# Kernel tuning notes

Measured on AMD Instinct MI355X. Metric: run time of the kernel, lower is better.

The kernel has to match this reference:

```python
import jax, jax.numpy as jnp
import numpy as np

# Junction-tree config: chain of NC cliques, each owning K new variables,
# parent separator = previous clique's K vars; S states per var; MLP hidden H.
B, NC, K, S, H = 512, 512, 4, 8, 128
D = 2 * K * S


def setup_inputs() -> dict:
    key = jax.random.key(0)
    ks = jax.random.split(key, 4)
    x = jax.random.randint(ks[0], (B, NC * K), 0, S, dtype=jnp.int32)
    sc = 0.05
    W1 = jax.random.normal(ks[1], (NC, D, H), jnp.float32) * sc
    b1 = jnp.zeros((NC, H), jnp.float32)
    W2 = jax.random.normal(ks[2], (NC, H, H), jnp.float32) * sc
    b2 = jnp.zeros((NC, H), jnp.float32)
    W3 = jax.random.normal(ks[3], (NC, H, S), jnp.float32) * sc
    b3 = jnp.zeros((NC, S), jnp.float32)
    return dict(x=x, W1=W1, b1=b1, W2=W2, b2=b2, W3=W3, b3=b3)


def reference(x, W1, b1, W2, b2, W3, b3):
    """fast_likelihood: per-clique log-prob [B, NC].

    Clique i owns vars [i*K,(i+1)*K); parent of clique i is clique i-1 (root=0
    conditions on a zero parent vector). Each clique runs a conditional
    autoregressive MLP over its K variables.
    """
    dtype = W1.dtype
    Bx = x.shape[0]
    xc = x.reshape(Bx, NC, K)                         # [B,NC,K] clique states
    oh = jax.nn.one_hot(xc, S, dtype=dtype)           # [B,NC,K,S]
    # Parent separator one-hot (root clique gets zeros) -> gather along tree.
    parent = jnp.concatenate([jnp.zeros_like(oh[:, :1]), oh[:, :-1]], axis=1)
    parent_flat = parent.reshape(Bx, NC, K * S)       # [B,NC,K*S]
    prefix_mask = (jnp.arange(K)[:, None] > jnp.arange(K)[None, :]).astype(dtype)  # [Kpos,Kvar]
    prefix = jnp.einsum('jk,bnks->bnjks', prefix_mask, oh).reshape(Bx, NC, K, K * S)
    inp = jnp.concatenate(
        [jnp.broadcast_to(parent_flat[:, :, None], prefix.shape), prefix], axis=-1
    )                                                 # [B,NC,K,D]
    h = jax.nn.relu(jnp.einsum('bnkd,ndh->bnkh', inp, W1) + b1[None, :, None])
    h = jax.nn.relu(jnp.einsum('bnkh,nhg->bnkg', h, W2) + b2[None, :, None])
    logits = jnp.einsum('bnkh,nhs->bnks', h, W3) + b3[None, :, None]
    logp = jax.nn.log_softmax(logits, axis=-1)        # [B,NC,K,S]
    logp_obs = jnp.take_along_axis(logp, xc[..., None], axis=-1)[..., 0]  # [B,NC,K]
    return logp_obs.sum(axis=-1)                      # [B,NC] per-clique logps
```

## Files before the change

kernel.cpp:

```cpp
#include <hip/hip_runtime.h>
#include <hip/hip_bf16.h>

typedef __bf16 bf16;
typedef __attribute__((ext_vector_type(4)))  __bf16 bf16x4;
typedef __attribute__((ext_vector_type(8)))  __bf16 bf16x8;
typedef __attribute__((ext_vector_type(16))) float  f32x16;

#define B_   512
#define NC_  512
#define K_   4
#define S_   8
#define H_   128
#define D_   64
#define XROW (NC_ * K_)
#define NITER 32

static __device__ __forceinline__ int swap23(int v) {
    return (v & ~12) | ((v & 4) << 1) | ((v & 8) >> 1);
}

__global__ __launch_bounds__(256, 2)
void jt_mlp_kernel(const int*   __restrict__ x,
                   const float* __restrict__ W1g, const float* __restrict__ b1g,
                   const float* __restrict__ W2g, const float* __restrict__ b2g,
                   const float* __restrict__ W3g, const float* __restrict__ b3g,
                   float* __restrict__ out)
{
    __shared__ __align__(16) bf16 SW2[128 * 128];
    __shared__ __align__(16) bf16 SWX[128 * 64];
    __shared__ __align__(16) bf16 SW3[8 * 128];
    __shared__ __align__(16) float LX[2][64][4];

    const int tid  = threadIdx.x;
    const int lane = tid & 63;
    const int w    = tid >> 6;
    const int pair = w >> 1;
    const int h    = w & 1;
    const int l31  = lane & 31;
    const int lhi  = lane >> 5;
    const int kk   = l31 & 3;
    const int n    = blockIdx.x;

    const float* W1p = W1g + (size_t)n * (D_ * H_);
    const float* W2p = W2g + (size_t)n * (H_ * H_);
    const float* W3p = W3g + (size_t)n * (H_ * S_);
    const float* b1p = b1g + n * H_;
    const float* b2p = b2g + n * H_;
    const float* b3p = b3g + n * S_;

    const int p31 = swap23(l31);
    const bf16 one = (bf16)1.0f, zero = (bf16)0.0f;

    {
        const int c0 = (tid & 31) * 4;
        const int k0 = (tid >> 5) * 8;
        float rows[8][4];
#pragma unroll
        for (int i = 0; i < 8; ++i) {
            float4 t4 = *(const float4*)(W1p + (k0 + i) * H_ + c0);
            if (n == 0 && k0 < 32) t4 = make_float4(0.f, 0.f, 0.f, 0.f);
            rows[i][0] = t4.x; rows[i][1] = t4.y; rows[i][2] = t4.z; rows[i][3] = t4.w;
        }
        if (k0 == 0) {
            const float4 bb = *(const float4*)(b1p + c0);
#pragma unroll
            for (int i = 0; i < 8; ++i) {
                rows[i][0] += bb.x; rows[i][1] += bb.y;
                rows[i][2] += bb.z; rows[i][3] += bb.w;
            }
        }
#pragma unroll
        for (int j2 = 0; j2 < 4; ++j2) {
            const int c = c0 + j2;
            const int p = (c & ~31) | swap23(c & 31);
            const int ch = (k0 >> 3) ^ (p & 7);
            bf16x4 lo, hi;
#pragma unroll
            for (int i = 0; i < 4; ++i) {
                lo[i] = (bf16)rows[i][j2];
                hi[i] = (bf16)rows[4 + i][j2];
            }
            *(bf16x4*)&SWX[p * 64 + ch * 8 + 0] = lo;
            *(bf16x4*)&SWX[p * 64 + ch * 8 + 4] = hi;
        }
    }
    {
        const int c0 = (tid & 31) * 4;
        const int kbase = (tid >> 5) * 16;
#pragma unroll
        for (int hh = 0; hh < 2; ++hh) {
            const int k0 = kbase + hh * 8;
            float rows[8][4];
#pragma unroll
            for (int i = 0; i < 8; ++i) {
                const float4 t4 = *(const float4*)(W2p + (k0 + i) * H_ + c0);
                rows[i][0] = t4.x; rows[i][1] = t4.y; rows[i][2] = t4.z; rows[i][3] = t4.w;
            }
#pragma unroll
            for (int j2 = 0; j2 < 4; ++j2) {
                const int c = c0 + j2;
                const int p = (c & ~31) | swap23(c & 31);
                const int ch = (k0 >> 3) ^ (p & 15) ^ ((p & 16) >> 2);
                bf16x4 lo, hi;
#pragma unroll
                for (int i = 0; i < 4; ++i) {
                    lo[i] = (bf16)rows[i][j2];
                    hi[i] = (bf16)rows[4 + i][j2];
                }
                *(bf16x4*)&SW2[p * 128 + ch * 8 + 0] = lo;
                *(bf16x4*)&SW2[p * 128 + ch * 8 + 4] = hi;
            }
        }
    }
    if (tid < 128) {
        const int s = tid >> 4, kc = tid & 15, k0 = kc * 8;
        float vv[8];
#pragma unroll
        for (int i = 0; i < 8; ++i) vv[i] = W3p[(k0 + i) * S_ + s];
        const int ch = kc ^ s;
        bf16x4 lo, hi;
#pragma unroll
        for (int i = 0; i < 4; ++i) { lo[i] = (bf16)vv[i]; hi[i] = (bf16)vv[4 + i]; }
        *(bf16x4*)&SW3[s * 128 + ch * 8 + 0] = lo;
        *(bf16x4*)&SW3[s * 128 + ch * 8 + 4] = hi;
    }
    __syncthreads();

    bf16x8 w1f[2][4];
#pragma unroll
    for (int aa = 0; aa < 2; ++aa)
#pragma unroll
        for (int kt = 0; kt < 4; ++kt)
            w1f[aa][kt] = *(const bf16x8*)
                &SWX[(32 * (2 * h + aa) + l31) * 64 + (((kt << 1) + lhi) ^ (l31 & 7)) * 8];
    const int s2 = l31 & 7;
    bf16x8 w3f[4];
#pragma unroll
    for (int tt = 0; tt < 4; ++tt)
        w3f[tt] = *(const bf16x8*)
            &SW3[s2 * 128 + ((((4 * h + tt) << 1) + lhi) ^ s2) * 8];
    bf16x8 w2b0, w2b1, onef;
#pragma unroll
    for (int j = 0; j < 8; ++j) { w2b0[j] = zero; w2b1[j] = zero; onef[j] = zero; }
    w2b0[0] = lhi ? zero : (bf16)b2p[32 * (2 * h + 0) + p31];
    w2b1[0] = lhi ? zero : (bf16)b2p[32 * (2 * h + 1) + p31];
    onef[0] = lhi ? zero : one;
    const float4 b3q = *(const float4*)(b3p + 4 * lhi);

    f32x16 zf;
#pragma unroll
    for (int i = 0; i < 16; ++i) zf[i] = 0.f;

    __syncthreads();
    bf16* HX = SWX;

    const int itbase = pair * 256 + (l31 >> 2);
    int4 xo_c, xp_c;
    {
        const int* xb = x + (size_t)itbase * XROW + n * K_;
        xo_c = *(const int4*)xb;
        xp_c = (n > 0) ? *(const int4*)(xb - K_) : make_int4(0, 0, 0, 0);
    }

#pragma unroll 1
    for (int c = 0; c < NITER; ++c) {
        const int item = itbase + c * 8;
        const int4 xo = xo_c, xp = xp_c;
        if (c < NITER - 1) {
            const int* xb = x + (size_t)(item + 8) * XROW + n * K_;
            xo_c = *(const int4*)xb;
            xp_c = (n > 0) ? *(const int4*)(xb - K_) : make_int4(0, 0, 0, 0);
        }

        int sel[4];
        sel[0] = (n > 0) ? (lhi ? xp.y : xp.x) : (lhi ? -1 : 0);
        sel[1] = (n > 0) ? (lhi ? xp.w : xp.z) : -1;
        sel[2] = (kk > (lhi ? 1 : 0)) ? (lhi ? xo.y : xo.x) : -1;
        sel[3] = (kk > (lhi ? 3 : 2)) ? (lhi ? xo.w : xo.z) : -1;

        f32x16 A0 = zf, A1 = zf;
#pragma unroll
        for (int kt = 0; kt < 4; ++kt) {
            bf16x8 bf1;
#pragma unroll
            for (int j = 0; j < 8; ++j) bf1[j] = (sel[kt] == j) ? one : zero;
            A0 = __builtin_amdgcn_mfma_f32_32x32x16_bf16(w1f[0][kt], bf1, A0, 0, 0, 0);
            A1 = __builtin_amdgcn_mfma_f32_32x32x16_bf16(w1f[1][kt], bf1, A1, 0, 0, 0);
        }

        bf16x8 hfo[4];
#pragma unroll
        for (int t = 0; t < 4; ++t) {
            const f32x16& S = (t < 2) ? A0 : A1;
#pragma unroll
            for (int j = 0; j < 8; ++j)
                hfo[t][j] = (bf16)fmaxf(S[8 * (t & 1) + j], 0.f);
            *(bf16x8*)&HX[(((pair << 1) + h) * 4 + t) * 512 + lane * 8] = hfo[t];
        }
        __syncthreads();

        f32x16 C0 = zf, C1 = zf;
        const int swz = (l31 & 15) ^ ((l31 & 16) >> 2);
        const int p0 = (64 * h + l31) * 128;
        const int p1 = (64 * h + 32 + l31) * 128;
#pragma unroll
        for (int tt = 0; tt < 4; ++tt) {
            const int chunk = (((4 * h + tt) << 1) + lhi) ^ swz;
            const bf16x8 f0 = *(const bf16x8*)&SW2[p0 + chunk * 8];
            const bf16x8 f1 = *(const bf16x8*)&SW2[p1 + chunk * 8];
            C0 = __builtin_amdgcn_mfma_f32_32x32x16_bf16(f0, hfo[tt], C0, 0, 0, 0);
            C1 = __builtin_amdgcn_mfma_f32_32x32x16_bf16(f1, hfo[tt], C1, 0, 0, 0);
        }
#pragma unroll
        for (int tt = 0; tt < 4; ++tt) {
            const bf16x8 hp = *(const bf16x8*)
                &HX[(((pair << 1) + (1 - h)) * 4 + tt) * 512 + lane * 8];
            const int chunk = (((4 * (1 - h) + tt) << 1) + lhi) ^ swz;
            const bf16x8 f0 = *(const bf16x8*)&SW2[p0 + chunk * 8];
            const bf16x8 f1 = *(const bf16x8*)&SW2[p1 + chunk * 8];
            C0 = __builtin_amdgcn_mfma_f32_32x32x16_bf16(f0, hp, C0, 0, 0, 0);
            C1 = __builtin_amdgcn_mfma_f32_32x32x16_bf16(f1, hp, C1, 0, 0, 0);
        }
        C0 = __builtin_amdgcn_mfma_f32_32x32x16_bf16(w2b0, onef, C0, 0, 0, 0);
        C1 = __builtin_amdgcn_mfma_f32_32x32x16_bf16(w2b1, onef, C1, 0, 0, 0);

        f32x16 L = zf;
#pragma unroll
        for (int tt = 0; tt < 4; ++tt) {
            bf16x8 hg;
            const f32x16& S = (tt < 2) ? C0 : C1;
#pragma unroll
            for (int j = 0; j < 8; ++j)
                hg[j] = (bf16)fmaxf(S[8 * (tt & 1) + j], 0.f);
            L = __builtin_amdgcn_mfma_f32_32x32x16_bf16(w3f[tt], hg, L, 0, 0, 0);
        }

        if (h == 1)
            *(float4*)&LX[pair][lane][0] = make_float4(L[0], L[1], L[2], L[3]);
        __syncthreads();
        if (h == 0) {
            const float4 Lp = *(const float4*)&LX[pair][lane][0];
            float Ls0 = L[0] + Lp.x + b3q.x;
            float Ls1 = L[1] + Lp.y + b3q.y;
            float Ls2 = L[2] + Lp.z + b3q.z;
            float Ls3 = L[3] + Lp.w + b3q.w;

            float m4 = fmaxf(fmaxf(Ls0, Ls1), fmaxf(Ls2, Ls3));
            const float mm = fmaxf(m4, __shfl_xor(m4, 32));
            float e = __expf(Ls0 - mm) + __expf(Ls1 - mm) +
                      __expf(Ls2 - mm) + __expf(Ls3 - mm);
            const float ssum = e + __shfl_xor(e, 32);

            const int xs = (kk & 2) ? ((kk & 1) ? xo.w : xo.z)
                                    : ((kk & 1) ? xo.y : xo.x);
            const float own = (xs & 2) ? ((xs & 1) ? Ls3 : Ls2)
                                       : ((xs & 1) ? Ls1 : Ls0);
            const float oth = __shfl_xor(own, 32);
            const float obs = ((xs >> 2) == lhi) ? own : oth;
            float lp = obs - mm - __logf(ssum);
            lp += __shfl_xor(lp, 1);
            lp += __shfl_xor(lp, 2);
            if (lhi == 0 && kk == 0)
                out[(size_t)item * NC_ + n] = lp;
        }
    }
}

extern "C" void kernel_launch(void* const* d_in, const int* in_sizes, int n_in,
                              void* d_out, int out_size, void* d_ws, size_t ws_size,
                              hipStream_t stream) {
    const int*   x  = (const int*)d_in[0];
    const float* W1 = (const float*)d_in[1];
    const float* b1 = (const float*)d_in[2];
    const float* W2 = (const float*)d_in[3];
    const float* b2 = (const float*)d_in[4];
    const float* W3 = (const float*)d_in[5];
    const float* b3 = (const float*)d_in[6];
    float* out = (float*)d_out;
    jt_mlp_kernel<<<dim3(NC_), 256, 0, stream>>>(x, W1, b1, W2, b2, W3, b3, out);
}
```

Before: 169.7 us.

## Give each wave a full 32-token slice instead of splitting hidden across wave pairs

```diff
diff --git a/kernel.cpp b/kernel.cpp
--- a/kernel.cpp
+++ b/kernel.cpp
@@ -13,7 +13,7 @@
 #define H_   128
 #define D_   64
 #define XROW (NC_ * K_)
-#define NITER 32
+#define NITER 16
 
 static __device__ __forceinline__ int swap23(int v) {
     return (v & ~12) | ((v & 4) << 1) | ((v & 8) >> 1);
@@ -29,13 +29,10 @@
     __shared__ __align__(16) bf16 SW2[128 * 128];
     __shared__ __align__(16) bf16 SWX[128 * 64];
     __shared__ __align__(16) bf16 SW3[8 * 128];
-    __shared__ __align__(16) float LX[2][64][4];
 
     const int tid  = threadIdx.x;
     const int lane = tid & 63;
     const int w    = tid >> 6;
-    const int pair = w >> 1;
-    const int h    = w & 1;
     const int l31  = lane & 31;
     const int lhi  = lane >> 5;
     const int kk   = l31 & 3;
@@ -126,35 +123,33 @@
     }
     __syncthreads();
 
-    bf16x8 w1f[2][4];
-#pragma unroll
-    for (int aa = 0; aa < 2; ++aa)
+    bf16x8 w1f[4][4];
+#pragma unroll
+    for (int aa = 0; aa < 4; ++aa)
 #pragma unroll
         for (int kt = 0; kt < 4; ++kt)
             w1f[aa][kt] = *(const bf16x8*)
-                &SWX[(32 * (2 * h + aa) + l31) * 64 + (((kt << 1) + lhi) ^ (l31 & 7)) * 8];
+                &SWX[(32 * aa + l31) * 64 + (((kt << 1) + lhi) ^ (l31 & 7)) * 8];
+
     const int s2 = l31 & 7;
-    bf16x8 w3f[4];
-#pragma unroll
-    for (int tt = 0; tt < 4; ++tt)
-        w3f[tt] = *(const bf16x8*)
-            &SW3[s2 * 128 + ((((4 * h + tt) << 1) + lhi) ^ s2) * 8];
-    bf16x8 w2b0, w2b1, onef;
-#pragma unroll
-    for (int j = 0; j < 8; ++j) { w2b0[j] = zero; w2b1[j] = zero; onef[j] = zero; }
-    w2b0[0] = lhi ? zero : (bf16)b2p[32 * (2 * h + 0) + p31];
-    w2b1[0] = lhi ? zero : (bf16)b2p[32 * (2 * h + 1) + p31];
+
+    bf16x8 w2b[4], onef;
+#pragma unroll
+    for (int j = 0; j < 8; ++j) onef[j] = zero;
     onef[0] = lhi ? zero : one;
+#pragma unroll
+    for (int aa = 0; aa < 4; ++aa) {
+#pragma unroll
+        for (int j = 0; j < 8; ++j) w2b[aa][j] = zero;
+        w2b[aa][0] = lhi ? zero : (bf16)b2p[32 * aa + p31];
+    }
     const float4 b3q = *(const float4*)(b3p + 4 * lhi);
 
     f32x16 zf;
 #pragma unroll
     for (int i = 0; i < 16; ++i) zf[i] = 0.f;
 
-    __syncthreads();
-    bf16* HX = SWX;
-
-    const int itbase = pair * 256 + (l31 >> 2);
+    const int itbase = w * 8 + (l31 >> 2);
     int4 xo_c, xp_c;
     {
         const int* xb = x + (size_t)itbase * XROW + n * K_;
@@ -162,12 +157,18 @@
         xp_c = (n > 0) ? *(const int4*)(xb - K_) : make_int4(0, 0, 0, 0);
     }
 
+    const int swz = (l31 & 15) ^ ((l31 & 16) >> 2);
+    const int pr0 = (     l31) * 128;
+    const int pr1 = (32 + l31) * 128;
+    const int pr2 = (64 + l31) * 128;
+    const int pr3 = (96 + l31) * 128;
+
 #pragma unroll 1
     for (int c = 0; c < NITER; ++c) {
-        const int item = itbase + c * 8;
+        const int item = itbase + c * 32;
         const int4 xo = xo_c, xp = xp_c;
         if (c < NITER - 1) {
-            const int* xb = x + (size_t)(item + 8) * XROW + n * K_;
+            const int* xb = x + (size_t)(item + 32) * XROW + n * K_;
             xo_c = *(const int4*)xb;
             xp_c = (n > 0) ? *(const int4*)(xb - K_) : make_int4(0, 0, 0, 0);
         }
@@ -178,7 +179,7 @@
         sel[2] = (kk > (lhi ? 1 : 0)) ? (lhi ? xo.y : xo.x) : -1;
         sel[3] = (kk > (lhi ? 3 : 2)) ? (lhi ? xo.w : xo.z) : -1;
 
-        f32x16 A0 = zf, A1 = zf;
+        f32x16 A0 = zf, A1 = zf, A2 = zf, A3 = zf;
 #pragma unroll
         for (int kt = 0; kt < 4; ++kt) {
             bf16x8 bf1;
@@ -186,64 +187,75 @@
             for (int j = 0; j < 8; ++j) bf1[j] = (sel[kt] == j) ? one : zero;
             A0 = __builtin_amdgcn_mfma_f32_32x32x16_bf16(w1f[0][kt], bf1, A0, 0, 0, 0);
             A1 = __builtin_amdgcn_mfma_f32_32x32x16_bf16(w1f[1][kt], bf1, A1, 0, 0, 0);
-        }
-
-        bf16x8 hfo[4];
-#pragma unroll
-        for (int t = 0; t < 4; ++t) {
-            const f32x16& S = (t < 2) ? A0 : A1;
+            A2 = __builtin_amdgcn_mfma_f32_32x32x16_bf16(w1f[2][kt], bf1, A2, 0, 0, 0);
+            A3 = __builtin_amdgcn_mfma_f32_32x32x16_bf16(w1f[3][kt], bf1, A3, 0, 0, 0);
+        }
+
+        bf16x8 hfo[8];
+#pragma unroll
+        for (int t = 0; t < 8; ++t) {
+            const f32x16& Sa = (t < 2) ? A0 : (t < 4) ? A1 : (t < 6) ? A2 : A3;
 #pragma unroll
             for (int j = 0; j < 8; ++j)
-                hfo[t][j] = (bf16)fmaxf(S[8 * (t & 1) + j], 0.f);
-            *(bf16x8*)&HX[(((pair << 1) + h) * 4 + t) * 512 + lane * 8] = hfo[t];
-        }
-        __syncthreads();
-
-        f32x16 C0 = zf, C1 = zf;
-        const int swz = (l31 & 15) ^ ((l31 & 16) >> 2);
-        const int p0 = (64 * h + l31) * 128;
-        const int p1 = (64 * h + 32 + l31) * 128;
-#pragma unroll
-        for (int tt = 0; tt < 4; ++tt) {
-            const int chunk = (((4 * h + tt) << 1) + lhi) ^ swz;
-            const bf16x8 f0 = *(const bf16x8*)&SW2[p0 + chunk * 8];
-            const bf16x8 f1 = *(const bf16x8*)&SW2[p1 + chunk * 8];
-            C0 = __builtin_amdgcn_mfma_f32_32x32x16_bf16(f0, hfo[tt], C0, 0, 0, 0);
-            C1 = __builtin_amdgcn_mfma_f32_32x32x16_bf16(f1, hfo[tt], C1, 0, 0, 0);
-        }
-#pragma unroll
-        for (int tt = 0; tt < 4; ++tt) {
-            const bf16x8 hp = *(const bf16x8*)
-                &HX[(((pair << 1) + (1 - h)) * 4 + tt) * 512 + lane * 8];
-            const int chunk = (((4 * (1 - h) + tt) << 1) + lhi) ^ swz;
-            const bf16x8 f0 = *(const bf16x8*)&SW2[p0 + chunk * 8];
-            const bf16x8 f1 = *(const bf16x8*)&SW2[p1 + chunk * 8];
-            C0 = __builtin_amdgcn_mfma_f32_32x32x16_bf16(f0, hp, C0, 0, 0, 0);
-            C1 = __builtin_amdgcn_mfma_f32_32x32x16_bf16(f1, hp, C1, 0, 0, 0);
-        }
-        C0 = __builtin_amdgcn_mfma_f32_32x32x16_bf16(w2b0, onef, C0, 0, 0, 0);
-        C1 = __builtin_amdgcn_mfma_f32_32x32x16_bf16(w2b1, onef, C1, 0, 0, 0);
+                hfo[t][j] = (bf16)fmaxf(Sa[8 * (t & 1) + j], 0.f);
+        }
 
         f32x16 L = zf;
-#pragma unroll
-        for (int tt = 0; tt < 4; ++tt) {
-            bf16x8 hg;
-            const f32x16& S = (tt < 2) ? C0 : C1;
-#pragma unroll
-            for (int j = 0; j < 8; ++j)
-                hg[j] = (bf16)fmaxf(S[8 * (tt & 1) + j], 0.f);
-            L = __builtin_amdgcn_mfma_f32_32x32x16_bf16(w3f[tt], hg, L, 0, 0, 0);
-        }
-
-        if (h == 1)
-            *(float4*)&LX[pair][lane][0] = make_float4(L[0], L[1], L[2], L[3]);
-        __syncthreads();
-        if (h == 0) {
-            const float4 Lp = *(const float4*)&LX[pair][lane][0];
-            float Ls0 = L[0] + Lp.x + b3q.x;
-            float Ls1 = L[1] + Lp.y + b3q.y;
-            float Ls2 = L[2] + Lp.z + b3q.z;
-            float Ls3 = L[3] + Lp.w + b3q.w;
+
+        {
+            f32x16 C0 = zf, C1 = zf;
+#pragma unroll
+            for (int q = 0; q < 8; ++q) {
+                const int chunk = ((q << 1) + lhi) ^ swz;
+                const bf16x8 f0 = *(const bf16x8*)&SW2[pr0 + chunk * 8];
+                const bf16x8 f1 = *(const bf16x8*)&SW2[pr1 + chunk * 8];
+                C0 = __builtin_amdgcn_mfma_f32_32x32x16_bf16(f0, hfo[q], C0, 0, 0, 0);
+                C1 = __builtin_amdgcn_mfma_f32_32x32x16_bf16(f1, hfo[q], C1, 0, 0, 0);
+            }
+            C0 = __builtin_amdgcn_mfma_f32_32x32x16_bf16(w2b[0], onef, C0, 0, 0, 0);
+            C1 = __builtin_amdgcn_mfma_f32_32x32x16_bf16(w2b[1], onef, C1, 0, 0, 0);
+#pragma unroll
+            for (int q = 0; q < 4; ++q) {
+                bf16x8 hg;
+                const f32x16& Sc = (q < 2) ? C0 : C1;
+#pragma unroll
+                for (int j = 0; j < 8; ++j)
+                    hg[j] = (bf16)fmaxf(Sc[8 * (q & 1) + j], 0.f);
+                const bf16x8 w3q = *(const bf16x8*)
+                    &SW3[s2 * 128 + (((q << 1) + lhi) ^ s2) * 8];
+                L = __builtin_amdgcn_mfma_f32_32x32x16_bf16(w3q, hg, L, 0, 0, 0);
+            }
+        }
+        {
+            f32x16 C2 = zf, C3 = zf;
+#pragma unroll
+            for (int q = 0; q < 8; ++q) {
+                const int chunk = ((q << 1) + lhi) ^ swz;
+                const bf16x8 f2 = *(const bf16x8*)&SW2[pr2 + chunk * 8];
+                const bf16x8 f3 = *(const bf16x8*)&SW2[pr3 + chunk * 8];
+                C2 = __builtin_amdgcn_mfma_f32_32x32x16_bf16(f2, hfo[q], C2, 0, 0, 0);
+                C3 = __builtin_amdgcn_mfma_f32_32x32x16_bf16(f3, hfo[q], C3, 0, 0, 0);
+            }
+            C2 = __builtin_amdgcn_mfma_f32_32x32x16_bf16(w2b[2], onef, C2, 0, 0, 0);
+            C3 = __builtin_amdgcn_mfma_f32_32x32x16_bf16(w2b[3], onef, C3, 0, 0, 0);
+#pragma unroll
+            for (int q = 4; q < 8; ++q) {
+                bf16x8 hg;
+                const f32x16& Sc = (q < 6) ? C2 : C3;
+#pragma unroll
+                for (int j = 0; j < 8; ++j)
+                    hg[j] = (bf16)fmaxf(Sc[8 * (q & 1) + j], 0.f);
+                const bf16x8 w3q = *(const bf16x8*)
+                    &SW3[s2 * 128 + (((q << 1) + lhi) ^ s2) * 8];
+                L = __builtin_amdgcn_mfma_f32_32x32x16_bf16(w3q, hg, L, 0, 0, 0);
+            }
+        }
+
+        {
+            const float Ls0 = L[0] + b3q.x;
+            const float Ls1 = L[1] + b3q.y;
+            const float Ls2 = L[2] + b3q.z;
+            const float Ls3 = L[3] + b3q.w;
 
             float m4 = fmaxf(fmaxf(Ls0, Ls1), fmaxf(Ls2, Ls3));
             const float mm = fmaxf(m4, __shfl_xor(m4, 32));
```

New measurement: 254.5 us. +49.9%, slower.

## Split each item group across four waves with 512-thread blocks

Applied to the files above, without the earlier changes.

```diff
diff --git a/kernel.cpp b/kernel.cpp
--- a/kernel.cpp
+++ b/kernel.cpp
@@ -19,7 +19,7 @@
     return (v & ~12) | ((v & 4) << 1) | ((v & 8) >> 1);
 }
 
-__global__ __launch_bounds__(256, 2)
+__global__ __launch_bounds__(512, 4)
 void jt_mlp_kernel(const int*   __restrict__ x,
                    const float* __restrict__ W1g, const float* __restrict__ b1g,
                    const float* __restrict__ W2g, const float* __restrict__ b2g,
@@ -29,13 +29,13 @@
     __shared__ __align__(16) bf16 SW2[128 * 128];
     __shared__ __align__(16) bf16 SWX[128 * 64];
     __shared__ __align__(16) bf16 SW3[8 * 128];
-    __shared__ __align__(16) float LX[2][64][4];
+    __shared__ __align__(16) float LX[2][3][64][4];
 
     const int tid  = threadIdx.x;
     const int lane = tid & 63;
-    const int w    = tid >> 6;
-    const int pair = w >> 1;
-    const int h    = w & 1;
+    const int ws   = __builtin_amdgcn_readfirstlane(tid >> 6);
+    const int g    = ws >> 2;
+    const int qs   = ws & 3;
     const int l31  = lane & 31;
     const int lhi  = lane >> 5;
     const int kk   = l31 & 3;
@@ -51,7 +51,7 @@
     const int p31 = swap23(l31);
     const bf16 one = (bf16)1.0f, zero = (bf16)0.0f;
 
-    {
+    if (tid < 256) {
         const int c0 = (tid & 31) * 4;
         const int k0 = (tid >> 5) * 8;
         float rows[8][4];
@@ -86,30 +86,26 @@
     }
     {
         const int c0 = (tid & 31) * 4;
-        const int kbase = (tid >> 5) * 16;
-#pragma unroll
-        for (int hh = 0; hh < 2; ++hh) {
-            const int k0 = kbase + hh * 8;
-            float rows[8][4];
-#pragma unroll
-            for (int i = 0; i < 8; ++i) {
-                const float4 t4 = *(const float4*)(W2p + (k0 + i) * H_ + c0);
-                rows[i][0] = t4.x; rows[i][1] = t4.y; rows[i][2] = t4.z; rows[i][3] = t4.w;
-            }
-#pragma unroll
-            for (int j2 = 0; j2 < 4; ++j2) {
-                const int c = c0 + j2;
-                const int p = (c & ~31) | swap23(c & 31);
-                const int ch = (k0 >> 3) ^ (p & 15) ^ ((p & 16) >> 2);
-                bf16x4 lo, hi;
-#pragma unroll
-                for (int i = 0; i < 4; ++i) {
-                    lo[i] = (bf16)rows[i][j2];
-                    hi[i] = (bf16)rows[4 + i][j2];
-                }
-                *(bf16x4*)&SW2[p * 128 + ch * 8 + 0] = lo;
-                *(bf16x4*)&SW2[p * 128 + ch * 8 + 4] = hi;
-            }
+        const int k0 = (tid >> 5) * 8;
+        float rows[8][4];
+#pragma unroll
+        for (int i = 0; i < 8; ++i) {
+            const float4 t4 = *(const float4*)(W2p + (k0 + i) * H_ + c0);
+            rows[i][0] = t4.x; rows[i][1] = t4.y; rows[i][2] = t4.z; rows[i][3] = t4.w;
+        }
+#pragma unroll
+        for (int j2 = 0; j2 < 4; ++j2) {
+            const int c = c0 + j2;
+            const int p = (c & ~31) | swap23(c & 31);
+            const int ch = (k0 >> 3) ^ (p & 15) ^ ((p & 16) >> 2);
+            bf16x4 lo, hi;
+#pragma unroll
+            for (int i = 0; i < 4; ++i) {
+                lo[i] = (bf16)rows[i][j2];
+                hi[i] = (bf16)rows[4 + i][j2];
+            }
+            *(bf16x4*)&SW2[p * 128 + ch * 8 + 0] = lo;
+            *(bf16x4*)&SW2[p * 128 + ch * 8 + 4] = hi;
         }
     }
     if (tid < 128) {
@@ -126,24 +122,21 @@
     }
     __syncthreads();
 
-    bf16x8 w1f[2][4];
-#pragma unroll
-    for (int aa = 0; aa < 2; ++aa)
-#pragma unroll
-        for (int kt = 0; kt < 4; ++kt)
-            w1f[aa][kt] = *(const bf16x8*)
-                &SWX[(32 * (2 * h + aa) + l31) * 64 + (((kt << 1) + lhi) ^ (l31 & 7)) * 8];
+    bf16x8 w1f[4];
+#pragma unroll
+    for (int kt = 0; kt < 4; ++kt)
+        w1f[kt] = *(const bf16x8*)
+            &SWX[(32 * qs + l31) * 64 + (((kt << 1) + lhi) ^ (l31 & 7)) * 8];
     const int s2 = l31 & 7;
-    bf16x8 w3f[4];
-#pragma unroll
-    for (int tt = 0; tt < 4; ++tt)
-        w3f[tt] = *(const bf16x8*)
-            &SW3[s2 * 128 + ((((4 * h + tt) << 1) + lhi) ^ s2) * 8];
-    bf16x8 w2b0, w2b1, onef;
-#pragma unroll
-    for (int j = 0; j < 8; ++j) { w2b0[j] = zero; w2b1[j] = zero; onef[j] = zero; }
-    w2b0[0] = lhi ? zero : (bf16)b2p[32 * (2 * h + 0) + p31];
-    w2b1[0] = lhi ? zero : (bf16)b2p[32 * (2 * h + 1) + p31];
+    bf16x8 w3f[2];
+#pragma unroll
+    for (int e = 0; e < 2; ++e)
+        w3f[e] = *(const bf16x8*)
+            &SW3[s2 * 128 + ((((2 * qs + e) << 1) + lhi) ^ s2) * 8];
+    bf16x8 w2b, onef;
+#pragma unroll
+    for (int j = 0; j < 8; ++j) { w2b[j] = zero; onef[j] = zero; }
+    w2b[0] = lhi ? zero : (bf16)b2p[32 * qs + p31];
     onef[0] = lhi ? zero : one;
     const float4 b3q = *(const float4*)(b3p + 4 * lhi);
 
@@ -154,7 +147,7 @@
     __syncthreads();
     bf16* HX = SWX;
 
-    const int itbase = pair * 256 + (l31 >> 2);
+    const int itbase = g * 8 + (l31 >> 2);
     int4 xo_c, xp_c;
     {
         const int* xb = x + (size_t)itbase * XROW + n * K_;
@@ -162,12 +155,16 @@
         xp_c = (n > 0) ? *(const int4*)(xb - K_) : make_int4(0, 0, 0, 0);
     }
 
+    const int swz = (l31 & 15) ^ ((l31 & 16) >> 2);
+    const int pq  = (32 * qs + l31) * 128;
+    const int g8  = g * 8;
+
 #pragma unroll 1
     for (int c = 0; c < NITER; ++c) {
-        const int item = itbase + c * 8;
+        const int item = itbase + c * 16;
         const int4 xo = xo_c, xp = xp_c;
         if (c < NITER - 1) {
-            const int* xb = x + (size_t)(item + 8) * XROW + n * K_;
+            const int* xb = x + (size_t)(item + 16) * XROW + n * K_;
             xo_c = *(const int4*)xb;
             xp_c = (n > 0) ? *(const int4*)(xb - K_) : make_int4(0, 0, 0, 0);
         }
@@ -178,72 +175,60 @@
         sel[2] = (kk > (lhi ? 1 : 0)) ? (lhi ? xo.y : xo.x) : -1;
         sel[3] = (kk > (lhi ? 3 : 2)) ? (lhi ? xo.w : xo.z) : -1;
 
-        f32x16 A0 = zf, A1 = zf;
+        f32x16 A = zf;
 #pragma unroll
         for (int kt = 0; kt < 4; ++kt) {
             bf16x8 bf1;
 #pragma unroll
             for (int j = 0; j < 8; ++j) bf1[j] = (sel[kt] == j) ? one : zero;
-            A0 = __builtin_amdgcn_mfma_f32_32x32x16_bf16(w1f[0][kt], bf1, A0, 0, 0, 0);
-            A1 = __builtin_amdgcn_mfma_f32_32x32x16_bf16(w1f[1][kt], bf1, A1, 0, 0, 0);
-        }
-
-        bf16x8 hfo[4];
-#pragma unroll
-        for (int t = 0; t < 4; ++t) {
-            const f32x16& S = (t < 2) ? A0 : A1;
+            A = __builtin_amdgcn_mfma_f32_32x32x16_bf16(w1f[kt], bf1, A, 0, 0, 0);
+        }
+
+        bf16x8 hfo[2];
+#pragma unroll
+        for (int e = 0; e < 2; ++e) {
 #pragma unroll
             for (int j = 0; j < 8; ++j)
-                hfo[t][j] = (bf16)fmaxf(S[8 * (t & 1) + j], 0.f);
-            *(bf16x8*)&HX[(((pair << 1) + h) * 4 + t) * 512 + lane * 8] = hfo[t];
+                hfo[e][j] = (bf16)fmaxf(A[8 * e + j], 0.f);
+            *(bf16x8*)&HX[(g8 + 2 * qs + e) * 512 + lane * 8] = hfo[e];
         }
         __syncthreads();
 
-        f32x16 C0 = zf, C1 = zf;
-        const int swz = (l31 & 15) ^ ((l31 & 16) >> 2);
-        const int p0 = (64 * h + l31) * 128;
-        const int p1 = (64 * h + 32 + l31) * 128;
-#pragma unroll
-        for (int tt = 0; tt < 4; ++tt) {
-            const int chunk = (((4 * h + tt) << 1) + lhi) ^ swz;
-            const bf16x8 f0 = *(const bf16x8*)&SW2[p0 + chunk * 8];
-            const bf16x8 f1 = *(const bf16x8*)&SW2[p1 + chunk * 8];
-            C0 = __builtin_amdgcn_mfma_f32_32x32x16_bf16(f0, hfo[tt], C0, 0, 0, 0);
-            C1 = __builtin_amdgcn_mfma_f32_32x32x16_bf16(f1, hfo[tt], C1, 0, 0, 0);
-        }
-#pragma unroll
-        for (int tt = 0; tt < 4; ++tt) {
-            const bf16x8 hp = *(const bf16x8*)
-                &HX[(((pair << 1) + (1 - h)) * 4 + tt) * 512 + lane * 8];
-            const int chunk = (((4 * (1 - h) + tt) << 1) + lhi) ^ swz;
-            const bf16x8 f0 = *(const bf16x8*)&SW2[p0 + chunk * 8];
-            const bf16x8 f1 = *(const bf16x8*)&SW2[p1 + chunk * 8];
-            C0 = __builtin_amdgcn_mfma_f32_32x32x16_bf16(f0, hp, C0, 0, 0, 0);
-            C1 = __builtin_amdgcn_mfma_f32_32x32x16_bf16(f1, hp, C1, 0, 0, 0);
-        }
-        C0 = __builtin_amdgcn_mfma_f32_32x32x16_bf16(w2b0, onef, C0, 0, 0, 0);
-        C1 = __builtin_amdgcn_mfma_f32_32x32x16_bf16(w2b1, onef, C1, 0, 0, 0);
+        f32x16 C = __builtin_amdgcn_mfma_f32_32x32x16_bf16(w2b, onef, zf, 0, 0, 0);
+#pragma unroll
+        for (int gc = 0; gc < 8; ++gc) {
+            bf16x8 hf;
+            if (qs == (gc >> 1)) {
+                hf = hfo[gc & 1];
+            } else {
+                hf = *(const bf16x8*)&HX[(g8 + gc) * 512 + lane * 8];
+            }
+            const int chunk = ((gc << 1) + lhi) ^ swz;
+            const bf16x8 f = *(const bf16x8*)&SW2[pq + chunk * 8];
+            C = __builtin_amdgcn_mfma_f32_32x32x16_bf16(f, hf, C, 0, 0, 0);
+        }
 
         f32x16 L = zf;
 #pragma unroll
-        for (int tt = 0; tt < 4; ++tt) {
+        for (int e = 0; e < 2; ++e) {
             bf16x8 hg;
-            const f32x16& S = (tt < 2) ? C0 : C1;
 #pragma unroll
             for (int j = 0; j < 8; ++j)
-                hg[j] = (bf16)fmaxf(S[8 * (tt & 1) + j], 0.f);
-            L = __builtin_amdgcn_mfma_f32_32x32x16_bf16(w3f[tt], hg, L, 0, 0, 0);
-        }
-
-        if (h == 1)
-            *(float4*)&LX[pair][lane][0] = make_float4(L[0], L[1], L[2], L[3]);
+                hg[j] = (bf16)fmaxf(C[8 * e + j], 0.f);
+            L = __builtin_amdgcn_mfma_f32_32x32x16_bf16(w3f[e], hg, L, 0, 0, 0);
+        }
+
+        if (qs != 0)
+            *(float4*)&LX[g][qs - 1][lane][0] = make_float4(L[0], L[1], L[2], L[3]);
         __syncthreads();
-        if (h == 0) {
-            const float4 Lp = *(const float4*)&LX[pair][lane][0];
-            float Ls0 = L[0] + Lp.x + b3q.x;
-            float Ls1 = L[1] + Lp.y + b3q.y;
-            float Ls2 = L[2] + Lp.z + b3q.z;
-            float Ls3 = L[3] + Lp.w + b3q.w;
+        if (qs == 0) {
+            const float4 P0 = *(const float4*)&LX[g][0][lane][0];
+            const float4 P1 = *(const float4*)&LX[g][1][lane][0];
+            const float4 P2 = *(const float4*)&LX[g][2][lane][0];
+            float Ls0 = L[0] + P0.x + P1.x + P2.x + b3q.x;
+            float Ls1 = L[1] + P0.y + P1.y + P2.y + b3q.y;
+            float Ls2 = L[2] + P0.z + P1.z + P2.z + b3q.z;
+            float Ls3 = L[3] + P0.w + P1.w + P2.w + b3q.w;
 
             float m4 = fmaxf(fmaxf(Ls0, Ls1), fmaxf(Ls2, Ls3));
             const float mm = fmaxf(m4, __shfl_xor(m4, 32));
@@ -277,5 +262,5 @@
     const float* W3 = (const float*)d_in[5];
     const float* b3 = (const float*)d_in[6];
     float* out = (float*)d_out;
-    jt_mlp_kernel<<<dim3(NC_), 256, 0, stream>>>(x, W1, b1, W2, b2, W3, b3, out);
+    jt_mlp_kernel<<<dim3(NC_), 512, 0, stream>>>(x, W1, b1, W2, b2, W3, b3, out);
 }
```

Result: slower. 181.9 us (+7.2%).
